# Optimization experiments

Hardware: AMD Instinct MI355X
Metric: run time of the kernel (lower is better)

## Reference

```python
import jax, jax.numpy as jnp
import numpy as np

B, T, D, H = 4, 2048, 512, 8
DH = D // H
SCALE = DH ** -0.5
CAUSAL = True


def setup_inputs() -> dict:
    key = jax.random.key(0)
    k1, k2, k3, k4 = jax.random.split(key, 4)
    x = jax.random.normal(k1, (B, T, D), dtype=jnp.float32)
    # realistic padding mask: each batch element has a random valid length
    lengths = jax.random.randint(k4, (B,), T // 2, T + 1)
    m = (jnp.arange(T)[None, :] < lengths[:, None]).astype(jnp.float32)[:, :, None]  # (B,T,1)
    w_qkv = jax.random.normal(k2, (D, 3 * D), dtype=jnp.float32) * (D ** -0.5)
    w_out = jax.random.normal(k3, (D, D), dtype=jnp.float32) * (D ** -0.5)
    b_out = jnp.zeros((D,), dtype=jnp.float32)
    return {"x": x, "m": m, "w_qkv": w_qkv, "w_out": w_out, "b_out": b_out}


def reference(x, m, w_qkv, w_out, b_out):
    qkv = x @ w_qkv
    q, k, v = jnp.split(qkv, 3, axis=-1)
    q = q.reshape(B, T, H, DH)
    k = k.reshape(B, T, H, DH)
    v = v.reshape(B, T, H, DH)
    # scores: (b,i,j,h), materialized like the torch module
    e = jnp.einsum('bihd,bjhd->bijh', q, k) * SCALE
    # key-padding mask (b,i,j)
    kpm = m[:, :, None, 0] * m[:, None, :, 0]
    if CAUSAL:
        kpm = jnp.tril(kpm)
    neg = -jnp.finfo(e.dtype).max
    e = jnp.where(kpm[..., None] == 0, neg, e)
    a = jax.nn.softmax(e, axis=2)
    o = jnp.einsum('bijh,bjhd->bihd', a, v).reshape(B, T, D)
    o = o @ w_out + b_out
    return o * m
```

## Files before the change

kernel.cpp:

```cpp
#include <hip/hip_runtime.h>
#include <hip/hip_bf16.h>

#define B_   4
#define T_   2048
#define D_   512
#define H_   8
#define DH_  64
#define BT_  (B_*T_)
#define N3D_ (3*D_)

typedef __bf16  bf16x8 __attribute__((ext_vector_type(8)));
typedef float   f32x4  __attribute__((ext_vector_type(4)));
typedef short   short8 __attribute__((ext_vector_type(8)));
typedef unsigned short u16;

#if defined(__has_builtin)
#if __has_builtin(__builtin_amdgcn_exp2f)
#define EXP2_OK 1
#endif
#endif
#ifndef EXP2_OK
#define EXP2_OK 0
#endif

#if EXP2_OK
#define QSCALE_F (0.125f * 1.44269504088896340736f)
static __device__ __forceinline__ float fastexp(float x) { return __builtin_amdgcn_exp2f(x); }
#else
#define QSCALE_F (0.125f)
static __device__ __forceinline__ float fastexp(float x) { return __expf(x); }
#endif

static __device__ __forceinline__ f32x4 fzero() { f32x4 z = {0.f,0.f,0.f,0.f}; return z; }

static __device__ __forceinline__ f32x4 mfma16(short8 a, short8 b, f32x4 c) {
  return __builtin_amdgcn_mfma_f32_16x16x32_bf16(
      __builtin_bit_cast(bf16x8, a), __builtin_bit_cast(bf16x8, b), c, 0, 0, 0);
}

static __device__ __forceinline__ int swz(int byteoff) {
  return byteoff ^ (((byteoff >> 7) & 7) << 4);
}

static __device__ __forceinline__ u16 bf16bits(float f) {
  __hip_bfloat16 h = __float2bfloat16(f);
  return *reinterpret_cast<u16*>(&h);
}

static __device__ __forceinline__ void gld_lds16(const void* g, void* l) {
  __builtin_amdgcn_global_load_lds(
      (const __attribute__((address_space(1))) void*)g,
      (__attribute__((address_space(3))) void*)l, 16, 0, 0);
}

#define XBLKS 768
__global__ __launch_bounds__(256) void prep_kernel(
    const float* __restrict__ x, const float* __restrict__ wqkv,
    const float* __restrict__ wout,
    u16* __restrict__ xb, u16* __restrict__ wqkvT, u16* __restrict__ woutT) {
  __shared__ u16 lt[64 * 72];
  const int tid = threadIdx.x;
  const int blk = blockIdx.x;

  if (blk < XBLKS) {
    const float4* x4 = reinterpret_cast<const float4*>(x);
    for (int idx = blk * 256 + tid; idx < BT_*D_/8; idx += XBLKS * 256) {
      float4 a = x4[idx*2], b = x4[idx*2+1];
      short8 o;
      o[0] = (short)bf16bits(a.x); o[1] = (short)bf16bits(a.y);
      o[2] = (short)bf16bits(a.z); o[3] = (short)bf16bits(a.w);
      o[4] = (short)bf16bits(b.x); o[5] = (short)bf16bits(b.y);
      o[6] = (short)bf16bits(b.z); o[7] = (short)bf16bits(b.w);
      *reinterpret_cast<short8*>(&xb[idx*8]) = o;
    }
    return;
  }

  int wb = blk - XBLKS;
  const float* src;
  u16* dst;
  int srcld, k0, n0;
  if (wb < 192) {
    src = wqkv; dst = wqkvT; srcld = N3D_;
    k0 = (wb & 7) * 64; n0 = (wb >> 3) * 64;
  } else {
    wb -= 192;
    src = wout; dst = woutT; srcld = D_;
    k0 = (wb & 7) * 64; n0 = (wb >> 3) * 64;
  }
  {
    int c = tid & 63, r0 = tid >> 6;
#pragma unroll
    for (int i = 0; i < 16; ++i) {
      int r = r0 * 16 + i;
      lt[r * 72 + c] = bf16bits(src[(long)(k0 + r) * srcld + n0 + c]);
    }
  }
  __syncthreads();
  {
    int kc = (tid & 7) * 8;
#pragma unroll
    for (int half = 0; half < 2; ++half) {
      int n = (tid >> 3) + half * 32;
      short8 v;
#pragma unroll
      for (int j = 0; j < 8; ++j) v[j] = (short)lt[(kc + j) * 72 + n];
      *reinterpret_cast<short8*>(&dst[(long)(n0 + n) * D_ + k0 + kc]) = v;
    }
  }
}

template <int MODE>
__global__ __launch_bounds__(256) void gemm_kernel(
    const u16* __restrict__ A, const u16* __restrict__ Wt,
    u16* __restrict__ qbuf, u16* __restrict__ kbuf, u16* __restrict__ vtbuf,
    const float* __restrict__ bias, const float* __restrict__ msk,
    float* __restrict__ out) {
  const int NBN = (MODE == 0) ? 12 : 4;
  const int lin = blockIdx.x;
  const int cpx = gridDim.x >> 3;
  const int nn = (lin & 7) * cpx + (lin >> 3);
  const int bm = nn / NBN, bn = nn % NBN;

  const int tid = threadIdx.x;
  const int w = tid >> 6, l = tid & 63;
  const int wr = w >> 1, wc = w & 1;
  const int lr = l & 15, lg = l >> 4;
  const int srow = l >> 3;
  const int scol = ((l & 7) ^ srow) << 4;

  __shared__ char ls[2][32768];

  f32x4 acc[4][4];
#pragma unroll
  for (int i = 0; i < 4; ++i)
#pragma unroll
    for (int j = 0; j < 4; ++j) acc[i][j] = fzero();

  const char* Ab = reinterpret_cast<const char*>(A) + (long)bm * 128 * 1024;
  const char* Wb = reinterpret_cast<const char*>(Wt) + (long)bn * 128 * 1024;

  auto stage = [&](int kt, char* dst) {
#pragma unroll
    for (int c = 0; c < 4; ++c) {
      int chunk = w * 4 + c;
      int row = chunk * 8 + srow;
      gld_lds16(Ab + (long)row * 1024 + kt * 128 + scol, dst + chunk * 1024);
      gld_lds16(Wb + (long)row * 1024 + kt * 128 + scol, dst + 16384 + chunk * 1024);
    }
  };

  stage(0, ls[0]);
  asm volatile("s_waitcnt vmcnt(0)" ::: "memory");
  __builtin_amdgcn_s_barrier();

  int cur = 0;
  for (int kt = 0; kt < 8; ++kt) {
    if (kt + 1 < 8) stage(kt + 1, ls[cur ^ 1]);
    const char* lsA = ls[cur];
    const char* lsB = ls[cur] + 16384;

#pragma unroll
    for (int c = 0; c < 2; ++c) {
      short8 af[4], bfr[4];
#pragma unroll
      for (int mi = 0; mi < 4; ++mi) {
        int row = wr * 64 + mi * 16 + lr;
        af[mi] = *reinterpret_cast<const short8*>(
            lsA + swz(row * 128 + c * 64 + lg * 16));
      }
#pragma unroll
      for (int ni = 0; ni < 4; ++ni) {
        int row = wc * 64 + ni * 16 + lr;
        bfr[ni] = *reinterpret_cast<const short8*>(
            lsB + swz(row * 128 + c * 64 + lg * 16));
      }
      __builtin_amdgcn_s_setprio(1);
#pragma unroll
      for (int mi = 0; mi < 4; ++mi)
#pragma unroll
        for (int ni = 0; ni < 4; ++ni)
          acc[mi][ni] = mfma16(af[mi], bfr[ni], acc[mi][ni]);
      __builtin_amdgcn_s_setprio(0);
    }

    asm volatile("s_waitcnt vmcnt(0)" ::: "memory");
    __builtin_amdgcn_s_barrier();
    cur ^= 1;
  }

  if (MODE == 0) {
    char* lse = ls[0];
    const int which = bn >> 2;
    if (which == 2) {
#pragma unroll
      for (int mi = 0; mi < 4; ++mi)
#pragma unroll
        for (int r = 0; r < 4; ++r) {
          int trow = wr * 64 + mi * 16 + lg * 4 + r;
#pragma unroll
          for (int ni = 0; ni < 4; ++ni) {
            int dcol = wc * 64 + ni * 16 + lr;
            int off = dcol * 256 + trow * 2;
            off ^= ((off >> 8) & 7) << 4;
            *reinterpret_cast<u16*>(lse + off) = bf16bits(acc[mi][ni][r]);
          }
        }
    } else {
      const float scale = (which == 0) ? QSCALE_F : 1.0f;
#pragma unroll
      for (int mi = 0; mi < 4; ++mi)
#pragma unroll
        for (int r = 0; r < 4; ++r) {
          int trow = wr * 64 + mi * 16 + lg * 4 + r;
#pragma unroll
          for (int ni = 0; ni < 4; ++ni) {
            int dcol = wc * 64 + ni * 16 + lr;
            int off = trow * 256 + dcol * 2;
            off ^= ((off >> 8) & 7) << 4;
            *reinterpret_cast<u16*>(lse + off) = bf16bits(acc[mi][ni][r] * scale);
          }
        }
    }
    __syncthreads();
    const int b = bm >> 4;
    const int tb0 = (bm & 15) * 128;
    if (which == 2) {
      const int bn8 = bn - 8;
#pragma unroll
      for (int it = 0; it < 8; ++it) {
        int dp = it * 16 + (tid >> 4);
        int tc = (tid & 15) * 16;
        int off = dp * 256 + (tc ^ ((dp & 7) << 4));
        short8 v = *reinterpret_cast<const short8*>(lse + off);
        int h = 2 * bn8 + (dp >> 6), d = dp & 63;
        long dst = ((long)((b * H_ + h) * DH_ + d)) * T_ + tb0 + tc / 2;
        *reinterpret_cast<short8*>(vtbuf + dst) = v;
      }
    } else {
      u16* obuf = (which == 0) ? qbuf : kbuf;
#pragma unroll
      for (int it = 0; it < 8; ++it) {
        int trow = it * 16 + (tid >> 4);
        int tc = (tid & 15) * 16;
        int off = trow * 256 + (tc ^ ((trow & 7) << 4));
        short8 v = *reinterpret_cast<const short8*>(lse + off);
        int dcol = tc / 2;
        int h = (bn & 3) * 2 + (dcol >> 6), d = dcol & 63;
        long dst = ((long)(b * H_ + h) * T_ + tb0 + trow) * DH_ + d;
        *reinterpret_cast<short8*>(obuf + dst) = v;
      }
    }
  } else {
#pragma unroll
    for (int mi = 0; mi < 4; ++mi) {
#pragma unroll
      for (int r = 0; r < 4; ++r) {
        int grow = bm * 128 + wr * 64 + mi * 16 + lg * 4 + r;
#pragma unroll
        for (int ni = 0; ni < 4; ++ni) {
          int gcol = bn * 128 + wc * 64 + ni * 16 + lr;
          float o = (acc[mi][ni][r] + bias[gcol]) * msk[grow];
          out[(long)grow * D_ + gcol] = o;
        }
      }
    }
  }
}

__global__ __launch_bounds__(512) void attn_kernel(
    const u16* __restrict__ q, const u16* __restrict__ k,
    const u16* __restrict__ vt, const float* __restrict__ msk,
    u16* __restrict__ ao) {
  const int bh = blockIdx.x;
  const int qt = 31 - blockIdx.y;
  const int b = bh >> 3, h = bh & 7;
  const int tid = threadIdx.x;
  const int w = tid >> 6;
  const int wq = w & 3;
  const int hf = w >> 2;
  const int l = tid & 63;
  const int lr = l & 15, lg = l >> 4;

  const float* mrow = msk + b * T_;

  unsigned long long bal = __ballot((l < 32) ? (mrow[l * 64] != 0.f) : false);
  const int nvalid = __popcll(bal);
  if (qt >= nvalid) return;
  const int nkv = (qt + 1 < nvalid) ? (qt + 1) : nvalid;
  const int nh = (nkv - hf + 1) >> 1;
  const int niter = (nkv + 1) >> 1;

  __shared__ char lsK[2 * 2 * 64 * 128];
  __shared__ char lsV[2 * 2 * 64 * 128];
  __shared__ char lsP[8 * 16 * 128];
  char* pbase = lsP + w * (16 * 128);
  char* myK = lsK + hf * 16384;
  char* myV = lsV + hf * 16384;

  const char* kb = reinterpret_cast<const char*>(k)  + (long)bh * T_ * 128;
  const char* vb = reinterpret_cast<const char*>(vt) + (long)bh * DH_ * T_ * 2;
  const char* qb = reinterpret_cast<const char*>(q);

  const int qrow0 = qt * 64 + wq * 16;

  short8 qf[2];
#pragma unroll
  for (int c = 0; c < 2; ++c)
    qf[c] = *reinterpret_cast<const short8*>(
        qb + (((long)bh * T_ + qrow0 + lr) * DH_ + c * 32 + lg * 8) * 2);

  const int srow = l >> 3;
  const int scol = ((l & 7) ^ srow) << 4;

  auto issue = [&](int kt_, int buf) {
#pragma unroll
    for (int c = 0; c < 2; ++c) {
      int chunk = wq * 2 + c;
      int row = chunk * 8 + srow;
      gld_lds16(kb + ((long)kt_ * 64 + row) * 128 + scol,
                myK + buf * 8192 + chunk * 1024);
      gld_lds16(vb + (long)row * (T_ * 2) + kt_ * 128 + scol,
                myV + buf * 8192 + chunk * 1024);
    }
  };

  if (0 < nh) issue(hf, 0);

  float mrun = -__builtin_inff(), lrun = 0.f;
  f32x4 oacc[4];
#pragma unroll
  for (int g = 0; g < 4; ++g) oacc[g] = fzero();

  for (int i = 0; i < niter; ++i) {
    __syncthreads();
    if (i + 1 < nh) issue(2 * (i + 1) + hf, (i + 1) & 1);
    if (i < nh) {
      const int kt = 2 * i + hf;
      const char* lk = myK + (i & 1) * 8192;
      const char* lv = myV + (i & 1) * 8192;

      f32x4 st[4];
      __builtin_amdgcn_s_setprio(1);
#pragma unroll
      for (int ni = 0; ni < 4; ++ni) {
        short8 kf0 = *reinterpret_cast<const short8*>(
            lk + swz((ni * 16 + lr) * 128 + lg * 16));
        short8 kf1 = *reinterpret_cast<const short8*>(
            lk + swz((ni * 16 + lr) * 128 + 64 + lg * 16));
        f32x4 z = fzero();
        z = mfma16(kf0, qf[0], z);
        z = mfma16(kf1, qf[1], z);
        st[ni] = z;
      }
      __builtin_amdgcn_s_setprio(0);

      const bool diag = (kt == qt);
      const bool needcm = (mrow[kt * 64 + 63] == 0.f);
      if (diag || needcm) {
#pragma unroll
        for (int ni = 0; ni < 4; ++ni)
#pragma unroll
          for (int r = 0; r < 4; ++r) {
            int jin = ni * 16 + lg * 4 + r;
            bool bad = (diag && jin > wq * 16 + lr) ||
                       (needcm && mrow[kt * 64 + jin] == 0.f);
            if (bad) st[ni][r] = -3.402823466e38f;
          }
      }

      float pmax = -3.402823466e38f;
#pragma unroll
      for (int ni = 0; ni < 4; ++ni)
#pragma unroll
        for (int r = 0; r < 4; ++r) pmax = fmaxf(pmax, st[ni][r]);
      pmax = fmaxf(pmax, __shfl_xor(pmax, 16));
      pmax = fmaxf(pmax, __shfl_xor(pmax, 32));

      if (!__all(pmax - mrun <= 8.f)) {
        float newm = fmaxf(mrun, pmax);
        float alpha = fastexp(mrun - newm);
        lrun *= alpha;
        mrun = newm;
#pragma unroll
        for (int rr = 0; rr < 4; ++rr) {
          float a = __shfl(alpha, lg * 4 + rr, 16);
#pragma unroll
          for (int g = 0; g < 4; ++g) oacc[g][rr] *= a;
        }
      }

      float p[4][4];
      float rs = 0.f;
#pragma unroll
      for (int ni = 0; ni < 4; ++ni)
#pragma unroll
        for (int r = 0; r < 4; ++r) {
          float pv = fastexp(st[ni][r] - mrun);
          p[ni][r] = pv;
          rs += pv;
        }
      rs += __shfl_xor(rs, 16);
      rs += __shfl_xor(rs, 32);
      lrun += rs;

#pragma unroll
      for (int ni = 0; ni < 4; ++ni)
#pragma unroll
        for (int rp = 0; rp < 2; ++rp) {
          unsigned lo = bf16bits(p[ni][2 * rp]);
          unsigned hi = bf16bits(p[ni][2 * rp + 1]);
          *reinterpret_cast<unsigned*>(
              pbase + swz(lr * 128 + ni * 32 + lg * 8 + rp * 4)) = lo | (hi << 16);
        }
      asm volatile("s_waitcnt lgkmcnt(0)" ::: "memory");

      __builtin_amdgcn_s_setprio(1);
#pragma unroll
      for (int c = 0; c < 2; ++c) {
        short8 pa = *reinterpret_cast<const short8*>(
            pbase + swz(lr * 128 + c * 64 + lg * 16));
#pragma unroll
        for (int g = 0; g < 4; ++g) {
          short8 vf = *reinterpret_cast<const short8*>(
              lv + swz((g * 16 + lr) * 128 + c * 64 + lg * 16));
          oacc[g] = mfma16(pa, vf, oacc[g]);
        }
      }
      __builtin_amdgcn_s_setprio(0);
    }
  }

  __syncthreads();
  float* mO  = reinterpret_cast<float*>(lsK);
  float* mML = reinterpret_cast<float*>(lsK + 4 * 4096);
  if (hf == 1) {
#pragma unroll
    for (int g = 0; g < 4; ++g)
#pragma unroll
      for (int rr = 0; rr < 4; ++rr)
        mO[wq * 1024 + (lg * 4 + rr) * 64 + g * 16 + lr] = oacc[g][rr];
    if (lg == 0) {
      mML[wq * 32 + lr * 2]     = mrun;
      mML[wq * 32 + lr * 2 + 1] = lrun;
    }
  }
  __syncthreads();
  if (hf == 0) {
    float m1 = mML[wq * 32 + lr * 2];
    float l1 = mML[wq * 32 + lr * 2 + 1];
    float M  = fmaxf(mrun, m1);
    float a0 = fastexp(mrun - M);
    float a1 = fastexp(m1 - M);
    float L  = a0 * lrun + a1 * l1;
#pragma unroll
    for (int rr = 0; rr < 4; ++rr) {
      int qrow = lg * 4 + rr;
      float a0r = __shfl(a0, qrow, 16);
      float a1r = __shfl(a1, qrow, 16);
      float Lr  = __shfl(L,  qrow, 16);
      float inv = 1.0f / Lr;
      int t = qrow0 + qrow;
#pragma unroll
      for (int g = 0; g < 4; ++g) {
        float o = a0r * oacc[g][rr] +
                  a1r * mO[wq * 1024 + qrow * 64 + g * 16 + lr];
        ao[((long)(b * T_ + t)) * D_ + h * 64 + g * 16 + lr] = bf16bits(o * inv);
      }
    }
  }
}

extern "C" void kernel_launch(void* const* d_in, const int* in_sizes, int n_in,
                              void* d_out, int out_size, void* d_ws,
                              size_t ws_size, hipStream_t stream) {
  const float* x    = (const float*)d_in[0];
  const float* msk  = (const float*)d_in[1];
  const float* wqkv = (const float*)d_in[2];
  const float* wout = (const float*)d_in[3];
  const float* bout = (const float*)d_in[4];
  float* out = (float*)d_out;

  char* ws = (char*)d_ws;
  u16* xb    = (u16*)(ws);
  u16* wqkvT = (u16*)(ws + 8388608);
  u16* woutT = (u16*)(ws + 9961472);
  u16* qbuf  = (u16*)(ws + 10485760);
  u16* kbuf  = (u16*)(ws + 18874368);
  u16* vtbuf = (u16*)(ws + 27262976);
  u16* ao    = (u16*)(ws + 35651584);

  prep_kernel<<<1024, 256, 0, stream>>>(x, wqkv, wout, xb, wqkvT, woutT);
  gemm_kernel<0><<<(N3D_ / 128) * (BT_ / 128), 256, 0, stream>>>(
      xb, wqkvT, qbuf, kbuf, vtbuf, nullptr, nullptr, nullptr);
  attn_kernel<<<dim3(B_ * H_, T_ / 64), 512, 0, stream>>>(
      qbuf, kbuf, vtbuf, msk, ao);
  gemm_kernel<1><<<(D_ / 128) * (BT_ / 128), 256, 0, stream>>>(
      ao, woutT, nullptr, nullptr, nullptr, bout, msk, out);
}
```

Baseline: 70.77 us.

## Deepen GEMM K pipeline to three in-flight stages with smaller K tiles

Replaces the double-buffered 128-byte K tile loop in the projection GEMM with a four-buffer ring of 64-byte K tiles, keeping three global-to-LDS loads in flight and waiting with partial vmcnt counts. It also changes the LDS layout and swizzle to pair rows into 128-byte lines. The aim is to hide global load latency better behind MFMA work. In exchange there are twice as many barriers per K sweep, and the loop is fully unrolled.

```diff
diff --git a/kernel.cpp b/kernel.cpp
--- a/kernel.cpp
+++ b/kernel.cpp
@@ -51,6 +51,11 @@
   __builtin_amdgcn_global_load_lds(
       (const __attribute__((address_space(1))) void*)g,
       (__attribute__((address_space(3))) void*)l, 16, 0, 0);
+}
+
+template <int N>
+static __device__ __forceinline__ void vwait() {
+  asm volatile("s_waitcnt vmcnt(%0)" :: "i"(N) : "memory");
 }
 
 #define XBLKS 768
@@ -126,10 +131,8 @@
   const int w = tid >> 6, l = tid & 63;
   const int wr = w >> 1, wc = w & 1;
   const int lr = l & 15, lg = l >> 4;
-  const int srow = l >> 3;
-  const int scol = ((l & 7) ^ srow) << 4;
-
-  __shared__ char ls[2][32768];
+
+  __shared__ char ls[4][16384];
 
   f32x4 acc[4][4];
 #pragma unroll
@@ -140,57 +143,63 @@
   const char* Ab = reinterpret_cast<const char*>(A) + (long)bm * 128 * 1024;
   const char* Wb = reinterpret_cast<const char*>(Wt) + (long)bn * 128 * 1024;
 
+  const int sg  = ((l >> 3) << 1) + ((l >> 2) & 1);
+  const int skb = (((l & 3) ^ ((l >> 3) & 3)) << 4);
+
   auto stage = [&](int kt, char* dst) {
 #pragma unroll
-    for (int c = 0; c < 4; ++c) {
-      int chunk = w * 4 + c;
-      int row = chunk * 8 + srow;
-      gld_lds16(Ab + (long)row * 1024 + kt * 128 + scol, dst + chunk * 1024);
-      gld_lds16(Wb + (long)row * 1024 + kt * 128 + scol, dst + 16384 + chunk * 1024);
+    for (int c = 0; c < 2; ++c) {
+      int chunk = w * 2 + c;
+      int g = chunk * 16 + sg;
+      gld_lds16(Ab + (long)g * 1024 + kt * 64 + skb, dst + chunk * 1024);
+      gld_lds16(Wb + (long)g * 1024 + kt * 64 + skb, dst + 8192 + chunk * 1024);
     }
   };
 
+  auto comp = [&](const char* base) {
+    const char* lsA = base;
+    const char* lsB = base + 8192;
+    short8 af[4], bfr[4];
+#pragma unroll
+    for (int mi = 0; mi < 4; ++mi) {
+      int g = wr * 64 + mi * 16 + lr;
+      af[mi] = *reinterpret_cast<const short8*>(
+          lsA + (g >> 1) * 128 + (g & 1) * 64 + ((lg ^ ((g >> 1) & 3)) << 4));
+    }
+#pragma unroll
+    for (int ni = 0; ni < 4; ++ni) {
+      int g = wc * 64 + ni * 16 + lr;
+      bfr[ni] = *reinterpret_cast<const short8*>(
+          lsB + (g >> 1) * 128 + (g & 1) * 64 + ((lg ^ ((g >> 1) & 3)) << 4));
+    }
+    __builtin_amdgcn_s_setprio(1);
+#pragma unroll
+    for (int mi = 0; mi < 4; ++mi)
+#pragma unroll
+      for (int ni = 0; ni < 4; ++ni)
+        acc[mi][ni] = mfma16(af[mi], bfr[ni], acc[mi][ni]);
+    __builtin_amdgcn_s_setprio(0);
+  };
+
   stage(0, ls[0]);
-  asm volatile("s_waitcnt vmcnt(0)" ::: "memory");
-  __builtin_amdgcn_s_barrier();
-
-  int cur = 0;
-  for (int kt = 0; kt < 8; ++kt) {
-    if (kt + 1 < 8) stage(kt + 1, ls[cur ^ 1]);
-    const char* lsA = ls[cur];
-    const char* lsB = ls[cur] + 16384;
-
-#pragma unroll
-    for (int c = 0; c < 2; ++c) {
-      short8 af[4], bfr[4];
-#pragma unroll
-      for (int mi = 0; mi < 4; ++mi) {
-        int row = wr * 64 + mi * 16 + lr;
-        af[mi] = *reinterpret_cast<const short8*>(
-            lsA + swz(row * 128 + c * 64 + lg * 16));
-      }
-#pragma unroll
-      for (int ni = 0; ni < 4; ++ni) {
-        int row = wc * 64 + ni * 16 + lr;
-        bfr[ni] = *reinterpret_cast<const short8*>(
-            lsB + swz(row * 128 + c * 64 + lg * 16));
-      }
-      __builtin_amdgcn_s_setprio(1);
-#pragma unroll
-      for (int mi = 0; mi < 4; ++mi)
-#pragma unroll
-        for (int ni = 0; ni < 4; ++ni)
-          acc[mi][ni] = mfma16(af[mi], bfr[ni], acc[mi][ni]);
-      __builtin_amdgcn_s_setprio(0);
-    }
-
-    asm volatile("s_waitcnt vmcnt(0)" ::: "memory");
-    __builtin_amdgcn_s_barrier();
-    cur ^= 1;
-  }
+  stage(1, ls[1]);
+  stage(2, ls[2]);
+
+#define GSTEP(T, NW) { \
+    vwait<NW>(); \
+    __builtin_amdgcn_s_barrier(); \
+    asm volatile("" ::: "memory"); \
+    if ((T) + 3 < 16) stage((T) + 3, ls[((T) + 3) & 3]); \
+    comp(ls[(T) & 3]); \
+  }
+  GSTEP(0, 8)  GSTEP(1, 8)  GSTEP(2, 8)  GSTEP(3, 8)
+  GSTEP(4, 8)  GSTEP(5, 8)  GSTEP(6, 8)  GSTEP(7, 8)
+  GSTEP(8, 8)  GSTEP(9, 8)  GSTEP(10, 8) GSTEP(11, 8)
+  GSTEP(12, 8) GSTEP(13, 8) GSTEP(14, 4) GSTEP(15, 0)
+#undef GSTEP
 
   if (MODE == 0) {
-    char* lse = ls[0];
+    char* lse = &ls[0][0];
     const int which = bn >> 2;
     if (which == 2) {
 #pragma unroll
```

Measured after the change: 71.21 us. About the same (+0.6%).

## Fuse fp32-to-bf16 conversion of x into QKV GEMM and skip padded row tiles

Applied to the files above, without the earlier changes.

Drops the separate pass that converts x to bf16. The QKV GEMM now loads fp32 x into registers, packs it to bf16 with v_cvt_pk_bf16_f32 and writes it to swizzled LDS, overlapping the next tile's load with the MFMA work. Both GEMMs also return early for 128-row tiles whose first row is masked out, and the output GEMM writes zeros for those tiles. This saves an 8MB write and reread plus the GEMM work on padded rows, at the cost of extra register pressure and a register-staged A path in place of direct-to-LDS DMA. The skip relies on padding being a suffix of each sequence and on 128-row tiles not straddling batches.

```diff
diff --git a/kernel.cpp b/kernel.cpp
--- a/kernel.cpp
+++ b/kernel.cpp
@@ -12,6 +12,7 @@
 typedef __bf16  bf16x8 __attribute__((ext_vector_type(8)));
 typedef float   f32x4  __attribute__((ext_vector_type(4)));
 typedef short   short8 __attribute__((ext_vector_type(8)));
+typedef unsigned uint4v __attribute__((ext_vector_type(4)));
 typedef unsigned short u16;
 
 #if defined(__has_builtin)
@@ -53,30 +54,17 @@
       (__attribute__((address_space(3))) void*)l, 16, 0, 0);
 }
 
-#define XBLKS 768
+template <int N>
+static __device__ __forceinline__ void vwait() {
+  asm volatile("s_waitcnt vmcnt(%0)" :: "i"(N) : "memory");
+}
+
 __global__ __launch_bounds__(256) void prep_kernel(
-    const float* __restrict__ x, const float* __restrict__ wqkv,
-    const float* __restrict__ wout,
-    u16* __restrict__ xb, u16* __restrict__ wqkvT, u16* __restrict__ woutT) {
+    const float* __restrict__ wqkv, const float* __restrict__ wout,
+    u16* __restrict__ wqkvT, u16* __restrict__ woutT) {
   __shared__ u16 lt[64 * 72];
   const int tid = threadIdx.x;
-  const int blk = blockIdx.x;
-
-  if (blk < XBLKS) {
-    const float4* x4 = reinterpret_cast<const float4*>(x);
-    for (int idx = blk * 256 + tid; idx < BT_*D_/8; idx += XBLKS * 256) {
-      float4 a = x4[idx*2], b = x4[idx*2+1];
-      short8 o;
-      o[0] = (short)bf16bits(a.x); o[1] = (short)bf16bits(a.y);
-      o[2] = (short)bf16bits(a.z); o[3] = (short)bf16bits(a.w);
-      o[4] = (short)bf16bits(b.x); o[5] = (short)bf16bits(b.y);
-      o[6] = (short)bf16bits(b.z); o[7] = (short)bf16bits(b.w);
-      *reinterpret_cast<short8*>(&xb[idx*8]) = o;
-    }
-    return;
-  }
-
-  int wb = blk - XBLKS;
+  int wb = blockIdx.x;
   const float* src;
   u16* dst;
   int srcld, k0, n0;
@@ -112,7 +100,8 @@
 
 template <int MODE>
 __global__ __launch_bounds__(256) void gemm_kernel(
-    const u16* __restrict__ A, const u16* __restrict__ Wt,
+    const float* __restrict__ xf, const u16* __restrict__ A,
+    const u16* __restrict__ Wt,
     u16* __restrict__ qbuf, u16* __restrict__ kbuf, u16* __restrict__ vtbuf,
     const float* __restrict__ bias, const float* __restrict__ msk,
     float* __restrict__ out) {
@@ -123,6 +112,17 @@
   const int bm = nn / NBN, bn = nn % NBN;
 
   const int tid = threadIdx.x;
+
+  if (msk[bm * 128] == 0.f) {
+    if (MODE == 1) {
+      long base = (long)bm * 128 * D_;
+      float4 z4 = make_float4(0.f, 0.f, 0.f, 0.f);
+      for (int i = tid; i < 128 * D_ / 4; i += 256)
+        *reinterpret_cast<float4*>(out + base + i * 4) = z4;
+    }
+    return;
+  }
+
   const int w = tid >> 6, l = tid & 63;
   const int wr = w >> 1, wc = w & 1;
   const int lr = l & 15, lg = l >> 4;
@@ -137,60 +137,127 @@
 #pragma unroll
     for (int j = 0; j < 4; ++j) acc[i][j] = fzero();
 
+  const float* Af = xf + (long)bm * 128 * 512;
   const char* Ab = reinterpret_cast<const char*>(A) + (long)bm * 128 * 1024;
   const char* Wb = reinterpret_cast<const char*>(Wt) + (long)bn * 128 * 1024;
 
-  auto stage = [&](int kt, char* dst) {
+  const int ar = tid >> 1;
+  const int ac = (tid & 1) * 32;
+  float4 areg[8];
+
+  auto loadA = [&](int kt) {
+    const float* s = Af + (long)ar * 512 + kt * 64 + ac;
+#pragma unroll
+    for (int j = 0; j < 8; ++j)
+      areg[j] = *reinterpret_cast<const float4*>(s + j * 4);
+  };
+  auto writeA = [&](char* dstA) {
+    unsigned u[16];
+#pragma unroll
+    for (int j = 0; j < 8; ++j) {
+      asm("v_cvt_pk_bf16_f32 %0, %1, %2"
+          : "=v"(u[2 * j]) : "v"(areg[j].x), "v"(areg[j].y));
+      asm("v_cvt_pk_bf16_f32 %0, %1, %2"
+          : "=v"(u[2 * j + 1]) : "v"(areg[j].z), "v"(areg[j].w));
+    }
+#pragma unroll
+    for (int j = 0; j < 4; ++j) {
+      uint4v v4;
+      v4[0] = u[4 * j]; v4[1] = u[4 * j + 1];
+      v4[2] = u[4 * j + 2]; v4[3] = u[4 * j + 3];
+      *reinterpret_cast<uint4v*>(dstA + swz(ar * 128 + ac * 2 + j * 16)) = v4;
+    }
+  };
+  auto stageB = [&](int kt, char* dst) {
 #pragma unroll
     for (int c = 0; c < 4; ++c) {
       int chunk = w * 4 + c;
-      int row = chunk * 8 + srow;
-      gld_lds16(Ab + (long)row * 1024 + kt * 128 + scol, dst + chunk * 1024);
-      gld_lds16(Wb + (long)row * 1024 + kt * 128 + scol, dst + 16384 + chunk * 1024);
+      int g = chunk * 8 + srow;
+      gld_lds16(Wb + (long)g * 1024 + kt * 128 + scol,
+                dst + 16384 + chunk * 1024);
     }
   };
-
-  stage(0, ls[0]);
-  asm volatile("s_waitcnt vmcnt(0)" ::: "memory");
-  __builtin_amdgcn_s_barrier();
+  auto stageA_dma = [&](int kt, char* dst) {
+#pragma unroll
+    for (int c = 0; c < 4; ++c) {
+      int chunk = w * 4 + c;
+      int g = chunk * 8 + srow;
+      gld_lds16(Ab + (long)g * 1024 + kt * 128 + scol, dst + chunk * 1024);
+    }
+  };
+
+  auto comp = [&](const char* base) {
+    const char* lsA = base;
+    const char* lsB = base + 16384;
+    short8 af[4], bfr[4];
+#pragma unroll
+    for (int mi = 0; mi < 4; ++mi) {
+      int g = wr * 64 + mi * 16 + lr;
+      af[mi] = *reinterpret_cast<const short8*>(
+          lsA + swz(g * 128 + 0 * 64 + lg * 16) + 0);
+      af[mi] = *reinterpret_cast<const short8*>(lsA + swz(g * 128 + lg * 16));
+    }
+#pragma unroll
+    for (int ni = 0; ni < 4; ++ni) {
+      int g = wc * 64 + ni * 16 + lr;
+      bfr[ni] = *reinterpret_cast<const short8*>(lsB + swz(g * 128 + lg * 16));
+    }
+#pragma unroll
+    for (int c = 0; c < 2; ++c) {
+      short8 afc[4], bfc[4];
+#pragma unroll
+      for (int mi = 0; mi < 4; ++mi) {
+        int g = wr * 64 + mi * 16 + lr;
+        afc[mi] = *reinterpret_cast<const short8*>(
+            lsA + swz(g * 128 + c * 64 + lg * 16));
+      }
+#pragma unroll
+      for (int ni = 0; ni < 4; ++ni) {
+        int g = wc * 64 + ni * 16 + lr;
+        bfc[ni] = *reinterpret_cast<const short8*>(
+            lsB + swz(g * 128 + c * 64 + lg * 16));
+      }
+      __builtin_amdgcn_s_setprio(1);
+#pragma unroll
+      for (int mi = 0; mi < 4; ++mi)
+#pragma unroll
+        for (int ni = 0; ni < 4; ++ni)
+          acc[mi][ni] = mfma16(afc[mi], bfc[ni], acc[mi][ni]);
+      __builtin_amdgcn_s_setprio(0);
+    }
+  };
+
+  if (MODE == 0) {
+    loadA(0);
+    stageB(0, ls[0]);
+    writeA(&ls[0][0]);
+    __syncthreads();
+  } else {
+    stageA_dma(0, ls[0]);
+    stageB(0, ls[0]);
+    vwait<0>();
+    __builtin_amdgcn_s_barrier();
+  }
 
   int cur = 0;
   for (int kt = 0; kt < 8; ++kt) {
-    if (kt + 1 < 8) stage(kt + 1, ls[cur ^ 1]);
-    const char* lsA = ls[cur];
-    const char* lsB = ls[cur] + 16384;
-
-#pragma unroll
-    for (int c = 0; c < 2; ++c) {
-      short8 af[4], bfr[4];
-#pragma unroll
-      for (int mi = 0; mi < 4; ++mi) {
-        int row = wr * 64 + mi * 16 + lr;
-        af[mi] = *reinterpret_cast<const short8*>(
-            lsA + swz(row * 128 + c * 64 + lg * 16));
-      }
-#pragma unroll
-      for (int ni = 0; ni < 4; ++ni) {
-        int row = wc * 64 + ni * 16 + lr;
-        bfr[ni] = *reinterpret_cast<const short8*>(
-            lsB + swz(row * 128 + c * 64 + lg * 16));
-      }
-      __builtin_amdgcn_s_setprio(1);
-#pragma unroll
-      for (int mi = 0; mi < 4; ++mi)
-#pragma unroll
-        for (int ni = 0; ni < 4; ++ni)
-          acc[mi][ni] = mfma16(af[mi], bfr[ni], acc[mi][ni]);
-      __builtin_amdgcn_s_setprio(0);
-    }
-
-    asm volatile("s_waitcnt vmcnt(0)" ::: "memory");
-    __builtin_amdgcn_s_barrier();
-    cur ^= 1;
+    const int ncur = cur ^ 1;
+    if (MODE == 0) {
+      if (kt + 1 < 8) { loadA(kt + 1); stageB(kt + 1, ls[ncur]); }
+      comp(ls[cur]);
+      if (kt + 1 < 8) writeA(&ls[ncur][0]);
+      __syncthreads();
+    } else {
+      if (kt + 1 < 8) { stageA_dma(kt + 1, ls[ncur]); stageB(kt + 1, ls[ncur]); }
+      comp(ls[cur]);
+      vwait<0>();
+      __builtin_amdgcn_s_barrier();
+    }
+    cur = ncur;
   }
 
   if (MODE == 0) {
-    char* lse = ls[0];
+    char* lse = &ls[0][0];
     const int which = bn >> 2;
     if (which == 2) {
 #pragma unroll
@@ -482,19 +549,18 @@
   float* out = (float*)d_out;
 
   char* ws = (char*)d_ws;
-  u16* xb    = (u16*)(ws);
-  u16* wqkvT = (u16*)(ws + 8388608);
-  u16* woutT = (u16*)(ws + 9961472);
-  u16* qbuf  = (u16*)(ws + 10485760);
-  u16* kbuf  = (u16*)(ws + 18874368);
-  u16* vtbuf = (u16*)(ws + 27262976);
-  u16* ao    = (u16*)(ws + 35651584);
-
-  prep_kernel<<<1024, 256, 0, stream>>>(x, wqkv, wout, xb, wqkvT, woutT);
+  u16* wqkvT = (u16*)(ws);
+  u16* woutT = (u16*)(ws + 1572864);
+  u16* qbuf  = (u16*)(ws + 2097152);
+  u16* kbuf  = (u16*)(ws + 10485760);
+  u16* vtbuf = (u16*)(ws + 18874368);
+  u16* ao    = (u16*)(ws + 27262976);
+
+  prep_kernel<<<256, 256, 0, stream>>>(wqkv, wout, wqkvT, woutT);
   gemm_kernel<0><<<(N3D_ / 128) * (BT_ / 128), 256, 0, stream>>>(
-      xb, wqkvT, qbuf, kbuf, vtbuf, nullptr, nullptr, nullptr);
+      x, nullptr, wqkvT, qbuf, kbuf, vtbuf, nullptr, msk, nullptr);
   attn_kernel<<<dim3(B_ * H_, T_ / 64), 512, 0, stream>>>(
       qbuf, kbuf, vtbuf, msk, ao);
   gemm_kernel<1><<<(D_ / 128) * (BT_ / 128), 256, 0, stream>>>(
-      ao, woutT, nullptr, nullptr, nullptr, bout, msk, out);
-}
+      nullptr, ao, woutT, nullptr, nullptr, nullptr, bout, msk, out);
+}
```

Measured after the change: 95.01 us (median of 2 runs). 1.34x slower.
